# Performance work log

Measured on AMD Instinct MI355X. Metric: run time of the kernel, lower is better.

## Reference

```python
import jax, jax.numpy as jnp
import numpy as np
import math

B, T_FUT, T_LOOK, D, H = 8, 512, 2048, 1024, 16
HD = D // H


def setup_inputs() -> dict:
    key = jax.random.key(0)
    ks = jax.random.split(key, 12)
    xav = 1.0 / math.sqrt(D)  # approx xavier_uniform scale for square [D,D]
    return {
        "encoded_representation": jax.random.normal(ks[0], (B, T_LOOK, D), jnp.float32),
        "future_queries": jax.random.normal(ks[1], (B, T_FUT, D), jnp.float32),
        "decoder_lengths": jax.random.randint(ks[2], (B,), 1, T_FUT + 1),
        "encoder_lengths": jax.random.randint(ks[3], (B,), 1, T_LOOK + 1),
        "wq_w": jax.random.normal(ks[4], (D, D), jnp.float32) * xav,
        "wq_b": jnp.zeros((D,), jnp.float32),
        "wk_w": jax.random.normal(ks[5], (D, D), jnp.float32) * xav,
        "wk_b": jnp.zeros((D,), jnp.float32),
        "wv_w": jax.random.normal(ks[6], (D, D), jnp.float32) * xav,
        "wv_b": jnp.zeros((D,), jnp.float32),
        "wo_w": jax.random.normal(ks[7], (D, D), jnp.float32) * xav,
        "wo_b": jnp.zeros((D,), jnp.float32),
    }


def reference(encoded_representation, future_queries, decoder_lengths, encoder_lengths,
              wq_w, wq_b, wk_w, wk_b, wv_w, wv_b, wo_w, wo_b):
    # variable-length padding mask: [B, 1, T_fut, T_look]
    dec_valid = jnp.arange(T_FUT)[None, :] < decoder_lengths[:, None]   # [B, T_fut]
    enc_valid = jnp.arange(T_LOOK)[None, :] < encoder_lengths[:, None]  # [B, T_look]
    mask = dec_valid[:, None, :, None] & enc_valid[:, None, None, :]

    # torch nn.Linear: y = x @ W^T + b
    Q = (future_queries @ wq_w.T + wq_b).reshape(B, T_FUT, H, HD)
    K = (encoded_representation @ wk_w.T + wk_b).reshape(B, T_LOOK, H, HD)
    V = (encoded_representation @ wv_w.T + wv_b).reshape(B, T_LOOK, H, HD)

    scores = jnp.einsum("bqhd,bkhd->bhqk", Q, K) / math.sqrt(HD)
    # NOTE: faithful to source, which fills masked positions with -1e-09 (not -1e9)
    scores = jnp.where(mask, scores, jnp.float32(-1e-09))
    probs = jax.nn.softmax(scores, axis=-1)

    attended = jnp.einsum("bhqk,bkhd->bqhd", probs, V).reshape(B, T_FUT, D)
    return attended @ wo_w.T + wo_b
```

## Files before the change

### kernel.cpp

```cpp
#include <hip/hip_runtime.h>

typedef __attribute__((ext_vector_type(4))) float f32x4;
typedef __attribute__((ext_vector_type(8))) short s16x8;

__device__ __forceinline__ ushort f2bf(float f) {
  unsigned u = __float_as_uint(f);
  return (ushort)((u + 0x7fffu + ((u >> 16) & 1u)) >> 16);
}

__global__ __launch_bounds__(256) void cvt_all(
    const float4* __restrict__ enc, const float4* __restrict__ fq,
    const float4* __restrict__ wq, const float4* __restrict__ wk,
    const float4* __restrict__ wv, const float4* __restrict__ wo,
    ushort* __restrict__ enc16, ushort* __restrict__ fq16,
    ushort* __restrict__ wq16, ushort* __restrict__ wk16,
    ushort* __restrict__ wv16, ushort* __restrict__ wo16) {
  const int stride = gridDim.x * 256;
  for (int i = blockIdx.x * 256 + threadIdx.x; i < 6291456; i += stride) {
    const float4* src;
    ushort* dst;
    int k;
    if (i < 4194304) {
      src = enc; dst = enc16; k = i;
    } else if (i < 5242880) {
      src = fq; dst = fq16; k = i - 4194304;
    } else {
      const int j = i - 5242880, sel = j >> 18;
      k = j & 262143;
      src = sel == 0 ? wq : sel == 1 ? wk : sel == 2 ? wv : wo;
      dst = sel == 0 ? wq16 : sel == 1 ? wk16 : sel == 2 ? wv16 : wo16;
    }
    float4 v = src[k];
    uint2 o;
    o.x = (unsigned)f2bf(v.x) | ((unsigned)f2bf(v.y) << 16);
    o.y = (unsigned)f2bf(v.z) | ((unsigned)f2bf(v.w) << 16);
    *(uint2*)(dst + (size_t)k * 4) = o;
  }
}

__device__ __forceinline__ void gload_lds16(const void* g, void* l) {
  __builtin_amdgcn_global_load_lds((const __attribute__((address_space(1))) void*)g,
                                   (__attribute__((address_space(3))) void*)l, 16, 0, 0);
}

__global__ __launch_bounds__(512, 1) void gemm256_fused(
    const ushort* __restrict__ enc16, const ushort* __restrict__ fq16,
    const ushort* __restrict__ Bkv, const ushort* __restrict__ Bq,
    const float* __restrict__ wk_b, const float* __restrict__ wv_b,
    const float* __restrict__ wq_b,
    ushort* __restrict__ Ko, ushort* __restrict__ Vt, ushort* __restrict__ Qo,
    float* __restrict__ Tsum, const int* __restrict__ dlen,
    const int* __restrict__ elen, float qscale) {
  __shared__ char lds[131072];
  const int tid = threadIdx.x;
  const int lane = tid & 63, wid = tid >> 6;
  const int g = lane >> 4, r = lane & 15;
  const int wm = wid >> 2, wn = wid & 3;
  const int bid = blockIdx.x;

  const ushort* Amat;
  const ushort* Bmat;
  int m0, n0, role;
  if (bid < 512) {
    const int xcd = bid & 7, inner = bid >> 3;
    m0 = (xcd * 8 + (inner & 7)) * 256;
    n0 = (inner >> 3) * 256;
    Amat = enc16;
    Bmat = Bkv;
    if (n0 < 1024) {
      role = 0;
      if ((m0 & 2047) >= elen[m0 >> 11]) return;
    } else {
      role = 1;
    }
  } else {
    const int q = bid - 512;
    m0 = (q & 15) * 256;
    n0 = (q >> 4) * 256;
    Amat = fq16;
    Bmat = Bq;
    role = 2;
    if ((m0 & 511) >= dlen[m0 >> 9]) return;
  }
  const size_t rowb = 2048;

  const int srow = tid >> 3;
  const int scb = (((tid & 7) ^ (srow & 7)) << 4);
  const char* Asrc = (const char*)Amat + (size_t)(m0 + srow) * rowb + scb;
  const char* Bsrc = (const char*)Bmat + (size_t)(n0 + srow) * rowb + scb;

  auto sAh = [&](int kt, int h) {
    char* d0 = lds + (kt & 1) * 32768 + h * 16384 + tid * 16;
    const char* s0 = Asrc + (size_t)(h * 128) * rowb + (size_t)kt * 128;
    gload_lds16(s0, d0);
    gload_lds16(s0 + (size_t)64 * rowb, d0 + 8192);
  };
  auto sBh = [&](int kt, int h) {
    char* d0 = lds + 65536 + (kt & 1) * 32768 + h * 16384 + tid * 16;
    const char* s0 = Bsrc + (size_t)(h * 128) * rowb + (size_t)kt * 128;
    gload_lds16(s0, d0);
    gload_lds16(s0 + (size_t)64 * rowb, d0 + 8192);
  };

  const int cb0 = (g * 16) ^ ((r & 7) << 4);
  const int cb1 = (64 + g * 16) ^ ((r & 7) << 4);

  f32x4 acc[8][4] = {};

  sAh(0, 0); sAh(0, 1); sBh(0, 0); sBh(0, 1); sBh(1, 0); sBh(1, 1);
  asm volatile("s_waitcnt vmcnt(4)" ::: "memory");
  __builtin_amdgcn_s_barrier();

#define MFMA_(a, b, c) __builtin_amdgcn_mfma_f32_16x16x32_bf16(a, b, c, 0, 0, 0)
#define PH(AB, Q, STAGE, WAIT)                                                 \
  {                                                                            \
    s16x8 aq0 = *(const s16x8*)(AB + (2 * (Q)) * 2048 + cb0);                  \
    s16x8 aq1 = *(const s16x8*)(AB + (2 * (Q)) * 2048 + cb1);                  \
    s16x8 aq2 = *(const s16x8*)(AB + (2 * (Q) + 1) * 2048 + cb0);              \
    s16x8 aq3 = *(const s16x8*)(AB + (2 * (Q) + 1) * 2048 + cb1);              \
    STAGE;                                                                     \
    __builtin_amdgcn_s_barrier();                                              \
    asm volatile("s_waitcnt lgkmcnt(0)" ::: "memory");                         \
    __builtin_amdgcn_sched_barrier(0);                                         \
    __builtin_amdgcn_s_setprio(1);                                             \
    _Pragma("unroll") for (int ni = 0; ni < 4; ++ni)                           \
        acc[2 * (Q)][ni] = MFMA_(aq0, bfr[ni][0], acc[2 * (Q)][ni]);           \
    _Pragma("unroll") for (int ni = 0; ni < 4; ++ni)                           \
        acc[2 * (Q) + 1][ni] = MFMA_(aq2, bfr[ni][0], acc[2 * (Q) + 1][ni]);   \
    _Pragma("unroll") for (int ni = 0; ni < 4; ++ni)                           \
        acc[2 * (Q)][ni] = MFMA_(aq1, bfr[ni][1], acc[2 * (Q)][ni]);           \
    _Pragma("unroll") for (int ni = 0; ni < 4; ++ni)                           \
        acc[2 * (Q) + 1][ni] = MFMA_(aq3, bfr[ni][1], acc[2 * (Q) + 1][ni]);   \
    __builtin_amdgcn_s_setprio(0);                                             \
    WAIT;                                                                      \
    __builtin_amdgcn_s_barrier();                                              \
  }
#define LOADB(BB)                                                              \
  _Pragma("unroll") for (int ni = 0; ni < 4; ++ni) {                           \
    bfr[ni][0] = *(const s16x8*)(BB + ni * 2048 + cb0);                        \
    bfr[ni][1] = *(const s16x8*)(BB + ni * 2048 + cb1);                        \
  }

  const int NIT = 8;
  const char* AbB = lds + wm * 16384 + r * 128;
  const char* BbB = lds + 65536 + (wn >> 1) * 16384 + (wn & 1) * 8192 + r * 128;

  for (int it = 0; it < NIT; ++it) {
    const bool st = (it + 1 < NIT);
    const int k1 = 2 * it + 1, k2 = 2 * it + 2, k3 = 2 * it + 3;
    s16x8 bfr[4][2];
    LOADB(BbB);
    PH(AbB, 0, sAh(k1, 0), );
    PH(AbB, 1, sAh(k1, 1), );
    PH(AbB, 2, if (st) sBh(k2, 0), );
    PH(AbB, 3, if (st) sBh(k2, 1),
       if (st) { asm volatile("s_waitcnt vmcnt(4)" ::: "memory"); } else {
         asm volatile("s_waitcnt vmcnt(0)" ::: "memory");
       });
    const char* Ab1 = AbB + 32768;
    const char* Bb1 = BbB + 32768;
    LOADB(Bb1);
    PH(Ab1, 0, if (st) sAh(k2, 0), );
    PH(Ab1, 1, if (st) sAh(k2, 1), );
    PH(Ab1, 2, if (st) sBh(k3, 0), );
    PH(Ab1, 3, if (st) sBh(k3, 1),
       if (st) { asm volatile("s_waitcnt vmcnt(4)" ::: "memory"); });
  }
#undef PH
#undef LOADB
#undef MFMA_

  if (role != 1) {
    ushort* C = (role == 2) ? Qo : Ko;
    const float* bias0 = (role == 2) ? wq_b : wk_b;
    const float sc = (role == 2) ? qscale : 1.0f;
#pragma unroll
    for (int ni = 0; ni < 4; ++ni) {
      const int col = wn * 64 + ni * 16 + r;
      const float bv = bias0[n0 + col];
#pragma unroll
      for (int i = 0; i < 8; ++i)
#pragma unroll
        for (int j = 0; j < 4; ++j) {
          const int row = wm * 128 + i * 16 + g * 4 + j;
          *(ushort*)(lds + ((row * 512 + col * 2) ^ (((row >> 2) & 7) << 4))) =
              f2bf((acc[i][ni][j] + bv) * sc);
        }
    }
    __syncthreads();
    const int c = tid & 31, r0 = tid >> 5;
#pragma unroll
    for (int u = 0; u < 16; ++u) {
      const int row = u * 16 + r0;
      s16x8 v = *(const s16x8*)(lds + ((row * 512 + c * 16) ^ (((row >> 2) & 7) << 4)));
      *(s16x8*)(C + (size_t)(m0 + row) * 1024 + n0 + c * 8) = v;
    }
  } else {
    const int nv0 = n0 - 1024;
    const int bb = m0 >> 11, tt0 = m0 & 2047;
#pragma unroll
    for (int ni = 0; ni < 4; ++ni) {
      const int nv = nv0 + wn * 64 + ni * 16 + r;
      const float bv = wv_b[nv];
#pragma unroll
      for (int qq = 0; qq < 2; ++qq) {
        float s = 0.0f;
#pragma unroll
        for (int ii = 0; ii < 4; ++ii)
#pragma unroll
          for (int j = 0; j < 4; ++j) s += acc[qq * 4 + ii][ni][j];
        s += __shfl_xor(s, 16);
        s += __shfl_xor(s, 32);
        if (g == 0) {
          const int gt = (m0 + (wm * 2 + qq) * 64) >> 6;
          Tsum[((size_t)((gt >> 5) * 16 + (nv >> 6)) * 33 + (gt & 31)) * 64 + (nv & 63)] =
              s + 64.0f * bv;
        }
      }
    }
#pragma unroll
    for (int ni = 0; ni < 4; ++ni) {
      const int rowl = wn * 64 + ni * 16 + r;
      const float bv = wv_b[nv0 + rowl];
#pragma unroll
      for (int i = 0; i < 8; ++i)
#pragma unroll
        for (int j = 0; j < 4; ++j) {
          const int coll = wm * 128 + i * 16 + g * 4 + j;
          *(ushort*)(lds + ((rowl * 512 + coll * 2) ^ ((rowl & 7) << 4))) =
              f2bf(acc[i][ni][j] + bv);
        }
    }
    __syncthreads();
    const int c = tid & 31, r0 = tid >> 5;
#pragma unroll
    for (int u = 0; u < 16; ++u) {
      const int row = u * 16 + r0;
      s16x8 v = *(const s16x8*)(lds + ((row * 512 + c * 16) ^ ((row & 7) << 4)));
      *(s16x8*)(Vt + ((size_t)bb * 1024 + nv0 + row) * 2048 + tt0 + c * 8) = v;
    }
  }
}

__global__ __launch_bounds__(256) void oproj(const ushort* __restrict__ A,
                                             const ushort* __restrict__ B,
                                             const float* __restrict__ bias,
                                             float* __restrict__ C, int M, int N, int K) {
  __shared__ ushort As[128 * 32];
  __shared__ ushort Bs[128 * 32];
  const int tid = threadIdx.x;
  const int lane = tid & 63, w = tid >> 6;
  const int g = lane >> 4, r = lane & 15;
  const int m0 = blockIdx.x * 128, n0 = blockIdx.y * 128;
  const int wm = (w >> 1) * 64, wn = (w & 1) * 64;

  const int srow = tid >> 2;
  const int scb = (tid & 3) * 16;
  const char* Ag = (const char*)(A + (size_t)(m0 + srow) * K) + scb;
  const char* Bg = (const char*)(B + (size_t)(n0 + srow) * K) + scb;
  char* AsB = (char*)As + (tid & 192) * 16;
  char* BsB = (char*)Bs + (tid & 192) * 16;
  const size_t rowskip = (size_t)64 * K * sizeof(ushort);

  f32x4 acc[4][4] = {};

  for (int k0 = 0; k0 < K; k0 += 32) {
    gload_lds16(Ag + (size_t)k0 * 2, AsB);
    gload_lds16(Ag + rowskip + (size_t)k0 * 2, AsB + 4096);
    gload_lds16(Bg + (size_t)k0 * 2, BsB);
    gload_lds16(Bg + rowskip + (size_t)k0 * 2, BsB + 4096);
    __syncthreads();
    s16x8 af[4], bf[4];
#pragma unroll
    for (int i = 0; i < 4; ++i) af[i] = *(const s16x8*)&As[(wm + i * 16 + r) * 32 + g * 8];
#pragma unroll
    for (int i = 0; i < 4; ++i) bf[i] = *(const s16x8*)&Bs[(wn + i * 16 + r) * 32 + g * 8];
#pragma unroll
    for (int mi = 0; mi < 4; ++mi)
#pragma unroll
      for (int ni = 0; ni < 4; ++ni)
        acc[mi][ni] =
            __builtin_amdgcn_mfma_f32_16x16x32_bf16(af[mi], bf[ni], acc[mi][ni], 0, 0, 0);
    __syncthreads();
  }

#pragma unroll
  for (int ni = 0; ni < 4; ++ni) {
    const int n = n0 + wn + ni * 16 + r;
    const float bv = bias[n];
#pragma unroll
    for (int mi = 0; mi < 4; ++mi) {
      const int mb = m0 + wm + mi * 16 + g * 4;
#pragma unroll
      for (int j = 0; j < 4; ++j)
        C[(size_t)(mb + j) * N + n] = acc[mi][ni][j] + bv;
    }
  }
}

__global__ __launch_bounds__(64) void vsuffix(float* __restrict__ T) {
  const int bh = blockIdx.x;
  const int d = threadIdx.x;
  float* p = T + (size_t)bh * 33 * 64 + d;
  float run = 0.0f;
  p[32 * 64] = 0.0f;
  for (int t = 31; t >= 0; --t) {
    run += p[t * 64];
    p[t * 64] = run;
  }
}

__device__ __forceinline__ ushort* swz(ushort* base, int row, int colb) {
  return (ushort*)((char*)base + row * 128 + (colb ^ ((row & 7) << 4)));
}

__global__ __launch_bounds__(256) void attn_fwd(
    const ushort* __restrict__ Q, const ushort* __restrict__ Km,
    const ushort* __restrict__ Vt, const float* __restrict__ Vsuf,
    const int* __restrict__ dlen, const int* __restrict__ elen,
    ushort* __restrict__ Oatt) {
  const int tid = threadIdx.x;
  const int lane = tid & 63, w = tid >> 6;
  const int g = lane >> 4, r = lane & 15;
  const int qt = blockIdx.x, b = blockIdx.y, h = blockIdx.z;
  const int dl = dlen[b], el = elen[b];
  const float* VS = Vsuf + (size_t)(b * 16 + h) * 33 * 64;

  if (qt * 64 >= dl) {
    const int qrow = qt * 64 + w * 16 + g * 4;
#pragma unroll
    for (int dt = 0; dt < 4; ++dt) {
      const ushort hv = f2bf(VS[dt * 16 + r] * (1.0f / 2048.0f));
#pragma unroll
      for (int j = 0; j < 4; ++j)
        Oatt[(size_t)(b * 512 + qrow + j) * 1024 + h * 64 + dt * 16 + r] = hv;
    }
    return;
  }

  __shared__ ushort Ks[64 * 64];
  __shared__ ushort Vs[64 * 64];
  __shared__ ushort Ps[4 * 16 * 64];
  ushort* PsW = Ps + w * 16 * 64;
  const int qbase = qt * 64 + w * 16;

  s16x8 qf[2];
  {
    const ushort* qp = Q + (size_t)(b * 512 + qbase + r) * 1024 + h * 64 + g * 8;
    qf[0] = *(const s16x8*)qp;
    qf[1] = *(const s16x8*)(qp + 32);
  }

  f32x4 o[4] = {};
  float lrow[4] = {0.0f, 0.0f, 0.0f, 0.0f};
  bool qok[4];
#pragma unroll
  for (int j = 0; j < 4; ++j) qok[j] = (qbase + g * 4 + j) < dl;

  const int sr = tid >> 3;
  const int sc8 = (tid & 7) * 8;
  const int scb = sc8 * 2;
  const ushort* Kg = Km + (size_t)(b * 2048 + sr) * 1024 + h * 64 + sc8;
  const ushort* Vg = Vt + ((size_t)b * 1024 + h * 64 + sr) * 2048 + sc8;

  const int t_last = (el - 1) >> 6;

  s16x8 pk0, pk1, pv0, pv1;
  {
    pk0 = *(const s16x8*)(Kg);
    pk1 = *(const s16x8*)(Kg + (size_t)32 * 1024);
    pv0 = *(const s16x8*)(Vg);
    pv1 = *(const s16x8*)(Vg + (size_t)32 * 2048);
  }

  for (int t = 0; t <= t_last; ++t) {
    *(s16x8*)swz(Ks, sr, scb) = pk0;
    *(s16x8*)swz(Ks, sr + 32, scb) = pk1;
    *(s16x8*)swz(Vs, sr, scb) = pv0;
    *(s16x8*)swz(Vs, sr + 32, scb) = pv1;
    __syncthreads();

    if (t < t_last) {
      const int kv0 = (t + 1) * 64;
      pk0 = *(const s16x8*)(Kg + (size_t)kv0 * 1024);
      pk1 = *(const s16x8*)(Kg + (size_t)(kv0 + 32) * 1024);
      pv0 = *(const s16x8*)(Vg + kv0);
      pv1 = *(const s16x8*)(Vg + (size_t)32 * 2048 + kv0);
    }

    const int kv0 = t * 64;
    float p[4][4];
#pragma unroll
    for (int nt = 0; nt < 4; ++nt) {
      f32x4 s = {};
      s16x8 kf0 = *(const s16x8*)swz(Ks, nt * 16 + r, g * 16);
      s16x8 kf1 = *(const s16x8*)swz(Ks, nt * 16 + r, 64 + g * 16);
      s = __builtin_amdgcn_mfma_f32_16x16x32_bf16(qf[0], kf0, s, 0, 0, 0);
      s = __builtin_amdgcn_mfma_f32_16x16x32_bf16(qf[1], kf1, s, 0, 0, 0);
      const bool kok = (kv0 + nt * 16 + r) < el;
#pragma unroll
      for (int j = 0; j < 4; ++j) {
        const float pe = __builtin_amdgcn_exp2f(s[j]);
        p[nt][j] = (kok && qok[j]) ? pe : 1.0f;
      }
    }
#pragma unroll
    for (int nt = 0; nt < 4; ++nt)
#pragma unroll
      for (int j = 0; j < 4; ++j) lrow[j] += p[nt][j];

#pragma unroll
    for (int nt = 0; nt < 4; ++nt) {
#pragma unroll
      for (int jp = 0; jp < 4; jp += 2) {
        unsigned pk;
        asm("v_cvt_pk_bf16_f32 %0, %1, %2" : "=v"(pk) : "v"(p[nt][jp]), "v"(p[nt][jp + 1]));
        *swz(PsW, g * 4 + jp, (nt * 16 + r) * 2) = (ushort)pk;
        *swz(PsW, g * 4 + jp + 1, (nt * 16 + r) * 2) = (ushort)(pk >> 16);
      }
    }

#pragma unroll
    for (int kc = 0; kc < 2; ++kc) {
      s16x8 pf = *(const s16x8*)swz(PsW, r, kc * 64 + g * 16);
#pragma unroll
      for (int dt = 0; dt < 4; ++dt) {
        s16x8 vf = *(const s16x8*)swz(Vs, dt * 16 + r, kc * 64 + g * 16);
        o[dt] = __builtin_amdgcn_mfma_f32_16x16x32_bf16(pf, vf, o[dt], 0, 0, 0);
      }
    }
    __syncthreads();
  }

  const float tailcnt = (float)(2048 - (t_last + 1) * 64);
  const float* VT = VS + (t_last + 1) * 64;
#pragma unroll
  for (int dt = 0; dt < 4; ++dt) {
    const float tv = VT[dt * 16 + r];
#pragma unroll
    for (int j = 0; j < 4; ++j) o[dt][j] += tv;
  }

  float inv[4];
#pragma unroll
  for (int j = 0; j < 4; ++j) {
    float s = lrow[j];
    s += __shfl_xor(s, 1);
    s += __shfl_xor(s, 2);
    s += __shfl_xor(s, 4);
    s += __shfl_xor(s, 8);
    inv[j] = 1.0f / (s + tailcnt);
  }
#pragma unroll
  for (int dt = 0; dt < 4; ++dt)
#pragma unroll
    for (int j = 0; j < 4; ++j)
      Oatt[(size_t)(b * 512 + qbase + g * 4 + j) * 1024 + h * 64 + dt * 16 + r] =
          f2bf(o[dt][j] * inv[j]);
}

extern "C" void kernel_launch(void* const* d_in, const int* in_sizes, int n_in,
                              void* d_out, int out_size, void* d_ws, size_t ws_size,
                              hipStream_t stream) {
  const float* enc  = (const float*)d_in[0];
  const float* fq   = (const float*)d_in[1];
  const int* dlen   = (const int*)d_in[2];
  const int* elen   = (const int*)d_in[3];
  const float* wq_w = (const float*)d_in[4];
  const float* wq_b = (const float*)d_in[5];
  const float* wk_w = (const float*)d_in[6];
  const float* wk_b = (const float*)d_in[7];
  const float* wv_w = (const float*)d_in[8];
  const float* wv_b = (const float*)d_in[9];
  const float* wo_w = (const float*)d_in[10];
  const float* wo_b = (const float*)d_in[11];

  char* ws = (char*)d_ws;
  ushort* enc16 = (ushort*)(ws + 0);
  ushort* fq16  = (ushort*)(ws + 33554432);
  ushort* attw  = (ushort*)(ws + 33554432);
  ushort* wq16  = (ushort*)(ws + 41943040);
  ushort* wk16  = (ushort*)(ws + 44040192);
  ushort* wv16  = (ushort*)(ws + 46137344);
  ushort* wo16  = (ushort*)(ws + 48234496);
  float*  Vsuf  = (float*)(ws + 50331648);
  ushort* Qw    = (ushort*)(ws + 52428800);
  ushort* Kw    = (ushort*)(ws + 60817408);
  ushort* Vtw   = (ushort*)(ws + 94371840);

  cvt_all<<<4096, 256, 0, stream>>>((const float4*)enc, (const float4*)fq,
                                    (const float4*)wq_w, (const float4*)wk_w,
                                    (const float4*)wv_w, (const float4*)wo_w,
                                    enc16, fq16, wq16, wk16, wv16, wo16);

  const float qscale = 0.125f * 1.44269504088896340736f;
  gemm256_fused<<<576, 512, 0, stream>>>(enc16, fq16, wk16, wq16, wk_b, wv_b, wq_b,
                                         Kw, Vtw, Qw, Vsuf, dlen, elen, qscale);
  vsuffix<<<128, 64, 0, stream>>>(Vsuf);

  attn_fwd<<<dim3(8, 8, 16), 256, 0, stream>>>(Qw, Kw, Vtw, Vsuf, dlen, elen, attw);

  oproj<<<dim3(32, 8), 256, 0, stream>>>(attw, wo16, wo_b, (float*)d_out, 4096, 1024, 1024);
}
```

Before: 195.6 us.

## Load K and V MFMA fragments directly from global memory, dropping LDS staging

```diff
diff --git a/kernel.cpp b/kernel.cpp
--- a/kernel.cpp
+++ b/kernel.cpp
@@ -338,8 +338,6 @@
     return;
   }
 
-  __shared__ ushort Ks[64 * 64];
-  __shared__ ushort Vs[64 * 64];
   __shared__ ushort Ps[4 * 16 * 64];
   ushort* PsW = Ps + w * 16 * 64;
   const int qbase = qt * 64 + w * 16;
@@ -357,44 +355,20 @@
 #pragma unroll
   for (int j = 0; j < 4; ++j) qok[j] = (qbase + g * 4 + j) < dl;
 
-  const int sr = tid >> 3;
-  const int sc8 = (tid & 7) * 8;
-  const int scb = sc8 * 2;
-  const ushort* Kg = Km + (size_t)(b * 2048 + sr) * 1024 + h * 64 + sc8;
-  const ushort* Vg = Vt + ((size_t)b * 1024 + h * 64 + sr) * 2048 + sc8;
+  const ushort* Kb = Km + (size_t)(b * 2048 + r) * 1024 + h * 64 + g * 8;
+  const ushort* Vb = Vt + ((size_t)b * 1024 + h * 64 + r) * 2048 + g * 8;
 
   const int t_last = (el - 1) >> 6;
 
-  s16x8 pk0, pk1, pv0, pv1;
-  {
-    pk0 = *(const s16x8*)(Kg);
-    pk1 = *(const s16x8*)(Kg + (size_t)32 * 1024);
-    pv0 = *(const s16x8*)(Vg);
-    pv1 = *(const s16x8*)(Vg + (size_t)32 * 2048);
-  }
-
   for (int t = 0; t <= t_last; ++t) {
-    *(s16x8*)swz(Ks, sr, scb) = pk0;
-    *(s16x8*)swz(Ks, sr + 32, scb) = pk1;
-    *(s16x8*)swz(Vs, sr, scb) = pv0;
-    *(s16x8*)swz(Vs, sr + 32, scb) = pv1;
-    __syncthreads();
-
-    if (t < t_last) {
-      const int kv0 = (t + 1) * 64;
-      pk0 = *(const s16x8*)(Kg + (size_t)kv0 * 1024);
-      pk1 = *(const s16x8*)(Kg + (size_t)(kv0 + 32) * 1024);
-      pv0 = *(const s16x8*)(Vg + kv0);
-      pv1 = *(const s16x8*)(Vg + (size_t)32 * 2048 + kv0);
-    }
-
     const int kv0 = t * 64;
     float p[4][4];
 #pragma unroll
     for (int nt = 0; nt < 4; ++nt) {
+      const ushort* kp = Kb + (size_t)(kv0 + nt * 16) * 1024;
+      s16x8 kf0 = *(const s16x8*)kp;
+      s16x8 kf1 = *(const s16x8*)(kp + 32);
       f32x4 s = {};
-      s16x8 kf0 = *(const s16x8*)swz(Ks, nt * 16 + r, g * 16);
-      s16x8 kf1 = *(const s16x8*)swz(Ks, nt * 16 + r, 64 + g * 16);
       s = __builtin_amdgcn_mfma_f32_16x16x32_bf16(qf[0], kf0, s, 0, 0, 0);
       s = __builtin_amdgcn_mfma_f32_16x16x32_bf16(qf[1], kf1, s, 0, 0, 0);
       const bool kok = (kv0 + nt * 16 + r) < el;
@@ -425,11 +399,10 @@
       s16x8 pf = *(const s16x8*)swz(PsW, r, kc * 64 + g * 16);
 #pragma unroll
       for (int dt = 0; dt < 4; ++dt) {
-        s16x8 vf = *(const s16x8*)swz(Vs, dt * 16 + r, kc * 64 + g * 16);
+        s16x8 vf = *(const s16x8*)(Vb + (size_t)(dt * 16) * 2048 + kv0 + kc * 32);
         o[dt] = __builtin_amdgcn_mfma_f32_16x16x32_bf16(pf, vf, o[dt], 0, 0, 0);
       }
     }
-    __syncthreads();
   }
 
   const float tailcnt = (float)(2048 - (t_last + 1) * 64);
```

New measurement: 343.3 us. 1.76x slower.
